# Kernel tuning notes

Measured on AMD Instinct MI355X. Metric: run time of the kernel, lower is better.

Reference implementation:

```python
import jax, jax.numpy as jnp
import numpy as np

B, L, D = 4, 2048, 1024
H = 16
DH = D // H  # 64


def setup_inputs() -> dict:
    key = jax.random.key(0)
    ks = jax.random.split(key, 12)
    inp = {
        "key": jax.random.normal(ks[0], (B, L, D), jnp.float32),
        "value": jax.random.normal(ks[1], (B, L, D), jnp.float32),
        "query": jax.random.normal(ks[2], (B, L, D), jnp.float32),
        # causal mask: True = masked out (matches masked_fill semantics)
        "mask": jnp.broadcast_to(jnp.triu(jnp.ones((L, L), jnp.bool_), k=1), (B, L, L)),
        "Wk": jax.random.normal(ks[3], (D, D), jnp.float32) * 0.02,
        "bk": jnp.zeros((D,), jnp.float32),
        "Wv": jax.random.normal(ks[4], (D, D), jnp.float32) * 0.02,
        "bv": jnp.zeros((D,), jnp.float32),
        "Wq": jax.random.normal(ks[5], (D, D), jnp.float32) * 0.02,
        "bq": jnp.zeros((D,), jnp.float32),
        "Wo": jax.random.normal(ks[6], (D, D), jnp.float32) * 0.02,
        "bo": jnp.zeros((D,), jnp.float32),
    }
    return inp


def _split_heads(x):
    # [B, L, D] -> [B, H, L, DH]
    b, l, _ = x.shape
    return x.reshape(b, l, H, DH).transpose(0, 2, 1, 3)


def reference(key, value, query, mask, Wk, bk, Wv, bv, Wq, bq, Wo, bo):
    b, lq, _ = query.shape
    k_up = _split_heads(key @ Wk + bk)      # [B,H,Lk,DH]
    v_up = _split_heads(value @ Wv + bv)    # [B,H,Lk,DH]
    q_up = _split_heads(query @ Wq + bq) / jnp.sqrt(jnp.float32(DH))
    scores = jnp.einsum("bhqd,bhkd->bhqk", q_up, k_up)
    scores = jnp.where(mask[:, None, :, :], jnp.float32(-1e18), scores)
    attn = jax.nn.softmax(scores, axis=-1)  # dropout = identity (eval)
    ctx = jnp.einsum("bhqk,bhkd->bhqd", attn, v_up)
    ctx = ctx.transpose(0, 2, 1, 3).reshape(b, lq, H * DH)
    output = ctx @ Wo + bo                  # [B,Lq,D]
    top_attn = attn[:, 0, :, :]             # [B,Lq,Lk]
    return output, top_attn
```

## Files before the change

### kernel.cpp

```cpp
#include <hip/hip_runtime.h>
#include <hip/hip_bf16.h>
#include <stdint.h>

typedef unsigned short u16;
typedef unsigned int u32;
typedef __attribute__((ext_vector_type(8))) short bf16x8;
typedef __attribute__((ext_vector_type(4))) float f32x4;
typedef __attribute__((address_space(1))) unsigned int as1u;
typedef __attribute__((address_space(3))) unsigned int as3u;

#define DEV __device__ __forceinline__

DEV u16 f2bf(float f) {
  union { float f; unsigned u; } v; v.f = f;
  unsigned r = v.u + 0x7FFFu + ((v.u >> 16) & 1u);
  return (u16)(r >> 16);
}

DEV u32 cvtpk(float lo, float hi) {
  u32 r;
  asm("v_cvt_pk_bf16_f32 %0, %1, %2" : "=v"(r) : "v"(lo), "v"(hi));
  return r;
}

DEV void gl_lds16(const void* g, void* l) {
  __builtin_amdgcn_global_load_lds(
      reinterpret_cast<as1u*>(reinterpret_cast<uintptr_t>(g)),
      reinterpret_cast<as3u*>(reinterpret_cast<uintptr_t>(l)), 16, 0, 0);
}

DEV int swzh(int r, int c) { return r * 64 + (c ^ ((r & 7) << 3)); }
DEV int swzf(int r, int c) { return r * 64 + (c ^ ((r & 7) << 2)); }

DEV int xcdswz512(int bid) { return ((bid & 7) << 6) | (bid >> 3); }

__global__ __launch_bounds__(256) void cvt3_k(const float* __restrict__ I0,
                                              const float* __restrict__ I1,
                                              const float* __restrict__ I2,
                                              u16* __restrict__ O0,
                                              u16* __restrict__ O1,
                                              u16* __restrict__ O2) {
  const int z = blockIdx.z;
  const float* in = z == 0 ? I0 : z == 1 ? I1 : I2;
  u16* out = z == 0 ? O0 : z == 1 ? O1 : O2;
  const int idx = blockIdx.x * 256 + threadIdx.x;
#pragma unroll
  for (int j = 0; j < 8; ++j) {
    const int i = j * 262144 + idx;
    float4 x = ((const float4*)in)[i];
    uint2 p;
    p.x = cvtpk(x.x, x.y);
    p.y = cvtpk(x.z, x.w);
    ((uint2*)out)[i] = p;
  }
}

__global__ __launch_bounds__(256) void wtrans4_k(
    const float* __restrict__ W0, const float* __restrict__ W1,
    const float* __restrict__ W2, const float* __restrict__ W3,
    u16* __restrict__ T0, u16* __restrict__ T1, u16* __restrict__ T2,
    u16* __restrict__ T3) {
  const int z = blockIdx.z;
  const float* W = z == 0 ? W0 : z == 1 ? W1 : z == 2 ? W2 : W3;
  u16* Wt = z == 0 ? T0 : z == 1 ? T1 : z == 2 ? T2 : T3;
  __shared__ float t[64][65];
  const int tid = threadIdx.x;
  const int n0 = blockIdx.x * 64, k0 = blockIdx.y * 64;
  const int c = tid & 63, r4 = tid >> 6;
#pragma unroll
  for (int i = 0; i < 16; ++i) {
    int r = r4 * 16 + i;
    t[r][c] = W[(size_t)(k0 + r) * 1024 + n0 + c];
  }
  __syncthreads();
#pragma unroll
  for (int i = 0; i < 16; ++i) {
    int r = r4 * 16 + i;
    Wt[(size_t)(n0 + r) * 1024 + k0 + c] = f2bf(t[c][r]);
  }
}

__global__ __launch_bounds__(256) void qkvgemm_k(
    const u16* __restrict__ Akey, const u16* __restrict__ Aval,
    const u16* __restrict__ Aqry, const u16* __restrict__ BtK,
    const u16* __restrict__ BtV, const u16* __restrict__ BtQ,
    const float* __restrict__ bk, const float* __restrict__ bv,
    const float* __restrict__ bq, u16* __restrict__ Kup, u16* __restrict__ Vt,
    u16* __restrict__ Qup, float qscale) {
  constexpr int K = 1024;
  const int z = blockIdx.z;
  const u16* Ah = z == 0 ? Akey : z == 1 ? Aval : Aqry;
  const u16* Bt = z == 0 ? BtK : z == 1 ? BtV : BtQ;
  const float* bias = z == 0 ? bk : z == 1 ? bv : bq;
  u16* Cp = z == 0 ? Kup : z == 1 ? Vt : Qup;
  const float scale = z == 2 ? qscale : 1.0f;

  __shared__ alignas(16) char smem[65536];

  const int tid = threadIdx.x;
  const int lane = tid & 63, wid = tid >> 6;
  const int swz = xcdswz512(blockIdx.x);
  const int brow = (swz >> 3) * 128;
  const int bcol = (swz & 7) * 128;
  const int wr = (wid >> 1) * 64, wc = (wid & 1) * 64;

  f32x4 acc[4][4] = {};

  auto stage = [&](int kt, int buf) {
#pragma unroll
    for (int i = 0; i < 4; ++i) {
      int row = i * 32 + (tid >> 3);
      const int sc = ((tid & 7) ^ (row & 7)) << 3;
      gl_lds16(Ah + (size_t)(brow + row) * K + kt + sc,
               smem + buf * 32768 + i * 4096 + wid * 1024);
      gl_lds16(Bt + (size_t)(bcol + row) * K + kt + sc,
               smem + buf * 32768 + 16384 + i * 4096 + wid * 1024);
    }
  };

  stage(0, 0);
  __syncthreads();

  int cur = 0;
  for (int kt = 0; kt < K; kt += 64) {
    if (kt + 64 < K) stage(kt + 64, cur ^ 1);
    const u16* Ash = (const u16*)(smem + cur * 32768);
    const u16* Bs = (const u16*)(smem + cur * 32768 + 16384);
#pragma unroll
    for (int kk = 0; kk < 2; ++kk) {
      const int kcol = kk * 32 + (lane >> 4) * 8;
      bf16x8 a[4], bfr[4];
#pragma unroll
      for (int m = 0; m < 4; ++m)
        a[m] = *(const bf16x8*)(Ash + swzh(wr + m * 16 + (lane & 15), kcol));
#pragma unroll
      for (int n = 0; n < 4; ++n)
        bfr[n] = *(const bf16x8*)(Bs + swzh(wc + n * 16 + (lane & 15), kcol));
#pragma unroll
      for (int m = 0; m < 4; ++m)
#pragma unroll
        for (int n = 0; n < 4; ++n)
          acc[m][n] = __builtin_amdgcn_mfma_f32_16x16x32_bf16(
              a[m], bfr[n], acc[m][n], 0, 0, 0);
    }
    __syncthreads();
    cur ^= 1;
  }

  const int g = lane >> 4;
  if (z == 1) {
    u16* T = (u16*)smem;
#pragma unroll
    for (int m = 0; m < 4; ++m) {
      const int row0 = wr + m * 16 + g * 4;
#pragma unroll
      for (int n = 0; n < 4; ++n) {
        const int col = wc + n * 16 + (lane & 15);
        const float bv2 = bias[bcol + col];
        uint2 p;
        p.x = cvtpk(acc[m][n][0] + bv2, acc[m][n][1] + bv2);
        p.y = cvtpk(acc[m][n][2] + bv2, acc[m][n][3] + bv2);
        *(uint2*)((char*)T + col * 256 + ((row0 * 2) ^ ((col & 7) << 4))) = p;
      }
    }
    __syncthreads();
    const int bI = brow >> 11, l0 = brow & 2047;
#pragma unroll
    for (int i = 0; i < 8; ++i) {
      const int rr = i * 16 + (tid >> 4);
      const int xb = (tid & 15) * 16;
      uint4 v = *(uint4*)((char*)T + rr * 256 + (xb ^ ((rr & 7) << 4)));
      const int colg = bcol + rr;
      const int hh = colg >> 6, dh = colg & 63;
      *(uint4*)(&Cp[((size_t)((bI << 4) + hh) * 64 + dh) * 2048 + l0 +
                    (xb >> 1)]) = v;
    }
  } else {
#pragma unroll
    for (int m = 0; m < 4; ++m) {
      const int row0 = brow + wr + m * 16 + (g << 2);
#pragma unroll
      for (int n = 0; n < 4; ++n) {
        const int col = bcol + wc + n * 16 + (lane & 15);
        const float bv2 = bias[col];
        const int h = col >> 6, dh = col & 63;
#pragma unroll
        for (int r = 0; r < 4; ++r) {
          const int row = row0 + r;
          const float val = (acc[m][n][r] + bv2) * scale;
          const int b = row >> 11, l = row & 2047;
          Cp[((size_t)((b << 4) + h) * 2048 + l) * 64 + dh] = f2bf(val);
        }
      }
    }
  }
}

__global__ __launch_bounds__(256) void outgemm_k(const u16* __restrict__ Ah,
                                                 const u16* __restrict__ Bt,
                                                 const float* __restrict__ bias,
                                                 float* __restrict__ Cp) {
  constexpr int K = 1024;
  __shared__ alignas(16) char smem[65536];

  const int tid = threadIdx.x;
  const int lane = tid & 63, wid = tid >> 6;
  const int swz = xcdswz512(blockIdx.x);
  const int brow = (swz >> 3) * 128;
  const int bcol = (swz & 7) * 128;
  const int wr = (wid >> 1) * 64, wc = (wid & 1) * 64;

  f32x4 acc[4][4] = {};

  auto stage = [&](int kt, int buf) {
#pragma unroll
    for (int i = 0; i < 4; ++i) {
      int row = i * 32 + (tid >> 3);
      const int sc = ((tid & 7) ^ (row & 7)) << 3;
      gl_lds16(Ah + (size_t)(brow + row) * K + kt + sc,
               smem + buf * 32768 + i * 4096 + wid * 1024);
      gl_lds16(Bt + (size_t)(bcol + row) * K + kt + sc,
               smem + buf * 32768 + 16384 + i * 4096 + wid * 1024);
    }
  };

  stage(0, 0);
  __syncthreads();

  int cur = 0;
  for (int kt = 0; kt < K; kt += 64) {
    if (kt + 64 < K) stage(kt + 64, cur ^ 1);
    const u16* Ash = (const u16*)(smem + cur * 32768);
    const u16* Bs = (const u16*)(smem + cur * 32768 + 16384);
#pragma unroll
    for (int kk = 0; kk < 2; ++kk) {
      const int kcol = kk * 32 + (lane >> 4) * 8;
      bf16x8 a[4], bfr[4];
#pragma unroll
      for (int m = 0; m < 4; ++m)
        a[m] = *(const bf16x8*)(Ash + swzh(wr + m * 16 + (lane & 15), kcol));
#pragma unroll
      for (int n = 0; n < 4; ++n)
        bfr[n] = *(const bf16x8*)(Bs + swzh(wc + n * 16 + (lane & 15), kcol));
#pragma unroll
      for (int m = 0; m < 4; ++m)
#pragma unroll
        for (int n = 0; n < 4; ++n)
          acc[m][n] = __builtin_amdgcn_mfma_f32_16x16x32_bf16(
              a[m], bfr[n], acc[m][n], 0, 0, 0);
    }
    __syncthreads();
    cur ^= 1;
  }

#pragma unroll
  for (int m = 0; m < 4; ++m) {
    const int row0 = brow + wr + m * 16 + ((lane >> 4) << 2);
#pragma unroll
    for (int n = 0; n < 4; ++n) {
      const int col = bcol + wc + n * 16 + (lane & 15);
      const float bv2 = bias[col];
#pragma unroll
      for (int r = 0; r < 4; ++r)
        Cp[(size_t)(row0 + r) * 1024 + col] = acc[m][n][r] + bv2;
    }
  }
}

__global__ __launch_bounds__(512, 6) void attn_k(const u16* __restrict__ Q,
                                                 const u16* __restrict__ K,
                                                 const u16* __restrict__ Vt,
                                                 u16* __restrict__ ctx,
                                                 float2* __restrict__ stats) {
  const int tid = threadIdx.x, lane = tid & 63, wid = tid >> 6;
  const int bh = blockIdx.x;
  const int qt = (int)(gridDim.y - 1) - (int)blockIdx.y;
  const int b = bh >> 4, h = bh & 15;
  const size_t base = (size_t)bh * 2048 * 64;

  __shared__ alignas(16) u16 Ks[2][4096], Vs[2][4096], Ps[8192];

  bf16x8 qf[2];
  {
    const u16* qp = Q + base +
                    (size_t)(qt * 128 + wid * 16 + (lane & 15)) * 64 +
                    ((lane >> 4) << 3);
    qf[0] = *(const bf16x8*)(qp);
    qf[1] = *(const bf16x8*)(qp + 32);
  }

  const int srow = tid >> 3;
  const int scol = ((tid & 7) ^ (srow & 7)) << 3;

  f32x4 acc_o[4] = {};
  float m_run = -1e30f, l_run = 0.f;
  const int q = qt * 128 + wid * 16 + (lane & 15);
  const int qminw = qt * 128 + wid * 16;
  const int qmaxw = qminw + 15;
  const int g = lane >> 4;
  const int rmask7 = lane & 7;

  const int NT = 2 * qt + 2;

  gl_lds16(K + base + (size_t)srow * 64 + scol, (char*)Ks + tid * 16);
  gl_lds16(Vt + base + (size_t)srow * 2048 + scol, (char*)Vs + tid * 16);
  __syncthreads();

  int cur = 0;
  for (int kt = 0; kt < NT; ++kt) {
    if (kt < NT - 1) {
      gl_lds16(K + base + (size_t)((kt + 1) * 64 + srow) * 64 + scol,
               (char*)Ks + (cur ^ 1) * 8192 + tid * 16);
      gl_lds16(Vt + base + (size_t)srow * 2048 + (kt + 1) * 64 + scol,
               (char*)Vs + (cur ^ 1) * 8192 + tid * 16);
    }

    if (kt * 64 <= qmaxw) {
      f32x4 s[4] = {};
#pragma unroll
      for (int kk = 0; kk < 2; ++kk) {
        const int kcb = kk * 64 + g * 16;
#pragma unroll
        for (int n = 0; n < 4; ++n) {
          const int row = n * 16 + (lane & 15);
          bf16x8 kf = *(const bf16x8*)((char*)Ks + cur * 8192 + row * 128 +
                                       (kcb ^ (rmask7 << 4)));
          s[n] = __builtin_amdgcn_mfma_f32_16x16x32_bf16(kf, qf[kk], s[n],
                                                         0, 0, 0);
        }
      }

      if (kt * 64 + 63 > qminw) {
        const int kb = kt * 64 + g * 4;
#pragma unroll
        for (int n = 0; n < 4; ++n)
#pragma unroll
          for (int r = 0; r < 4; ++r)
            if (kb + n * 16 + r > q) s[n][r] = -1e30f;
      }

      float mx = s[0][0];
#pragma unroll
      for (int n = 0; n < 4; ++n)
#pragma unroll
        for (int r = 0; r < 4; ++r) mx = fmaxf(mx, s[n][r]);
      mx = fmaxf(mx, __shfl_xor(mx, 16, 64));
      mx = fmaxf(mx, __shfl_xor(mx, 32, 64));

      if (__any(mx - m_run > 8.0f)) {
        const float mn = fmaxf(m_run, mx);
        const float alpha = exp2f(m_run - mn);
        m_run = mn;
        l_run *= alpha;
#pragma unroll
        for (int r = 0; r < 4; ++r) {
          const float ar = __shfl(alpha, (g << 2) + r, 64);
#pragma unroll
          for (int n = 0; n < 4; ++n) acc_o[n][r] *= ar;
        }
      }

      float rs = 0.f;
#pragma unroll
      for (int n = 0; n < 4; ++n)
#pragma unroll
        for (int r = 0; r < 4; ++r) {
          const float pv = exp2f(s[n][r] - m_run);
          s[n][r] = pv;
          rs += pv;
        }
      rs += __shfl_xor(rs, 16, 64);
      rs += __shfl_xor(rs, 32, 64);
      l_run += rs;

#pragma unroll
      for (int n = 0; n < 4; ++n) {
        union { u32 w[2]; uint2 u; } pk;
        pk.w[0] = cvtpk(s[n][0], s[n][1]);
        pk.w[1] = cvtpk(s[n][2], s[n][3]);
        *(uint2*)((char*)Ps + wid * 2048 + (lane & 15) * 128 +
                  ((n * 32 + g * 8) ^ (rmask7 << 4))) = pk.u;
      }
      asm volatile("s_waitcnt lgkmcnt(0)" ::: "memory");

#pragma unroll
      for (int kk = 0; kk < 2; ++kk) {
        const int kcb = kk * 64 + g * 16;
        bf16x8 pf = *(const bf16x8*)((char*)Ps + wid * 2048 +
                                     (lane & 15) * 128 + (kcb ^ (rmask7 << 4)));
#pragma unroll
        for (int n = 0; n < 4; ++n) {
          const int row = n * 16 + (lane & 15);
          bf16x8 vf = *(const bf16x8*)((char*)Vs + cur * 8192 + row * 128 +
                                       (kcb ^ (rmask7 << 4)));
          acc_o[n] = __builtin_amdgcn_mfma_f32_16x16x32_bf16(pf, vf, acc_o[n],
                                                             0, 0, 0);
        }
      }
    }
    __syncthreads();
    cur ^= 1;
  }

  float linv[4];
#pragma unroll
  for (int r = 0; r < 4; ++r)
    linv[r] = 1.0f / __shfl(l_run, (g << 2) + r, 64);
#pragma unroll
  for (int r = 0; r < 4; ++r) {
    const int qo = qt * 128 + wid * 16 + (g << 2) + r;
#pragma unroll
    for (int n = 0; n < 4; ++n) {
      const int dh = n * 16 + (lane & 15);
      ctx[((size_t)(b * 2048 + qo)) * 1024 + h * 64 + dh] =
          f2bf(acc_o[n][r] * linv[r]);
    }
  }
  if (h == 0 && g == 0)
    stats[b * 2048 + q] = make_float2(m_run, l_run);
}

__global__ __launch_bounds__(256) void probs_k(const u16* __restrict__ Q,
                                               const u16* __restrict__ K,
                                               const float2* __restrict__ stats,
                                               float* __restrict__ out) {
  const int tid = threadIdx.x, lane = tid & 63, wid = tid >> 6;
  const int kt2 = blockIdx.x, qt = blockIdx.y, b = blockIdx.z;
  const int q0 = qt * 64, c0 = kt2 * 128;
  float* ot = out + ((size_t)b * 2048 + q0) * 2048 + c0;

  if (c0 > q0 + 63) {
    const float4 z = make_float4(0.f, 0.f, 0.f, 0.f);
#pragma unroll
    for (int i = 0; i < 8; ++i) {
      const int idx = i * 256 + tid;
      *(float4*)(ot + (size_t)(idx >> 5) * 2048 + ((idx & 31) << 2)) = z;
    }
    return;
  }

  __shared__ alignas(16) u16 Qs[4096], Ks2[8192];
  const size_t base = (size_t)(b * 16) * 2048 * 64;
#pragma unroll
  for (int i = 0; i < 2; ++i) {
    int row = i * 32 + (tid >> 3);
    gl_lds16(Q + base + (size_t)(q0 + row) * 64 + (((tid & 7) ^ (row & 7)) << 3),
             (char*)Qs + i * 4096 + wid * 1024);
  }
#pragma unroll
  for (int i = 0; i < 4; ++i) {
    int row = i * 32 + (tid >> 3);
    gl_lds16(K + base + (size_t)(c0 + row) * 64 + (((tid & 7) ^ (row & 7)) << 3),
             (char*)Ks2 + i * 4096 + wid * 1024);
  }
  __syncthreads();

  f32x4 s[8] = {};
#pragma unroll
  for (int kk = 0; kk < 2; ++kk) {
    const int kc = kk * 32 + (lane >> 4) * 8;
    bf16x8 aq = *(const bf16x8*)(Qs + swzh(wid * 16 + (lane & 15), kc));
#pragma unroll
    for (int n = 0; n < 8; ++n) {
      bf16x8 bk = *(const bf16x8*)(Ks2 + swzh(n * 16 + (lane & 15), kc));
      s[n] = __builtin_amdgcn_mfma_f32_16x16x32_bf16(aq, bk, s[n], 0, 0, 0);
    }
  }

#pragma unroll
  for (int r = 0; r < 4; ++r) {
    const int q = q0 + wid * 16 + ((lane >> 4) << 2) + r;
    const float2 st = stats[b * 2048 + q];
    const float rl = 1.0f / st.y;
#pragma unroll
    for (int n = 0; n < 8; ++n) {
      const int kp = c0 + n * 16 + (lane & 15);
      out[((size_t)b * 2048 + q) * 2048 + kp] =
          (kp <= q) ? exp2f(s[n][r] - st.x) * rl : 0.f;
    }
  }
}

extern "C" void kernel_launch(void* const* d_in, const int* in_sizes, int n_in,
                              void* d_out, int out_size, void* d_ws,
                              size_t ws_size, hipStream_t stream) {
  (void)in_sizes; (void)n_in; (void)out_size; (void)ws_size;
  const float* key = (const float*)d_in[0];
  const float* value = (const float*)d_in[1];
  const float* query = (const float*)d_in[2];
  const float* Wk = (const float*)d_in[4];
  const float* bk = (const float*)d_in[5];
  const float* Wv = (const float*)d_in[6];
  const float* bv = (const float*)d_in[7];
  const float* Wq = (const float*)d_in[8];
  const float* bq = (const float*)d_in[9];
  const float* Wo = (const float*)d_in[10];
  const float* bo = (const float*)d_in[11];

  char* ws = (char*)d_ws;
  u16* WtK = (u16*)(ws);
  u16* WtV = (u16*)(ws + (2u << 20));
  u16* WtQ = (u16*)(ws + (4u << 20));
  u16* WtO = (u16*)(ws + (6u << 20));
  u16* Kup = (u16*)(ws + (8u << 20));
  u16* Qup = (u16*)(ws + (24u << 20));
  u16* Vt  = (u16*)(ws + (40u << 20));
  u16* ctx = (u16*)(ws + (56u << 20));
  float2* stats = (float2*)(ws + (72u << 20));
  u16* Akb = (u16*)(ws + (76u << 20));
  u16* Avb = (u16*)(ws + (92u << 20));
  u16* Aqb = (u16*)(ws + (108u << 20));

  wtrans4_k<<<dim3(16, 16, 4), 256, 0, stream>>>(Wk, Wv, Wq, Wo, WtK, WtV,
                                                 WtQ, WtO);
  cvt3_k<<<dim3(1024, 1, 3), 256, 0, stream>>>(key, value, query, Akb, Avb,
                                               Aqb);

  const float qscale = 0.125f * 1.44269504088896340736f;
  qkvgemm_k<<<dim3(512, 1, 3), 256, 0, stream>>>(
      Akb, Avb, Aqb, WtK, WtV, WtQ, bk, bv, bq, Kup, Vt, Qup, qscale);

  attn_k<<<dim3(64, 16), 512, 0, stream>>>(Qup, Kup, Vt, ctx, stats);

  float* out = (float*)d_out;
  probs_k<<<dim3(16, 32, 4), 256, 0, stream>>>(Qup, Kup, stats,
                                               out + (size_t)8388608);

  outgemm_k<<<512, 256, 0, stream>>>(ctx, WtO, bo, out);
}
```

Measured before the change: 206.3 us.

## Use 128-wide KV tiles in attention and compute row sums via MFMA

```diff
diff --git a/kernel.cpp b/kernel.cpp
--- a/kernel.cpp
+++ b/kernel.cpp
@@ -30,7 +30,6 @@
 }
 
 DEV int swzh(int r, int c) { return r * 64 + (c ^ ((r & 7) << 3)); }
-DEV int swzf(int r, int c) { return r * 64 + (c ^ ((r & 7) << 2)); }
 
 DEV int xcdswz512(int bid) { return ((bid & 7) << 6) | (bid >> 3); }
 
@@ -267,18 +266,18 @@
   }
 }
 
-__global__ __launch_bounds__(512, 6) void attn_k(const u16* __restrict__ Q,
+__global__ __launch_bounds__(512, 4) void attn_k(const u16* __restrict__ Q,
                                                  const u16* __restrict__ K,
                                                  const u16* __restrict__ Vt,
                                                  u16* __restrict__ ctx,
                                                  float2* __restrict__ stats) {
   const int tid = threadIdx.x, lane = tid & 63, wid = tid >> 6;
   const int bh = blockIdx.x;
-  const int qt = (int)(gridDim.y - 1) - (int)blockIdx.y;
+  const int qt = 15 - (int)blockIdx.y;
   const int b = bh >> 4, h = bh & 15;
   const size_t base = (size_t)bh * 2048 * 64;
 
-  __shared__ alignas(16) u16 Ks[2][4096], Vs[2][4096], Ps[8192];
+  __shared__ alignas(16) u16 Ks[2][8192], Vs[2][8192], Ps[8192];
 
   bf16x8 qf[2];
   {
@@ -288,136 +287,147 @@
     qf[0] = *(const bf16x8*)(qp);
     qf[1] = *(const bf16x8*)(qp + 32);
   }
-
-  const int srow = tid >> 3;
-  const int scol = ((tid & 7) ^ (srow & 7)) << 3;
-
-  f32x4 acc_o[4] = {};
-  float m_run = -1e30f, l_run = 0.f;
+  bf16x8 ones;
+#pragma unroll
+  for (int i = 0; i < 8; ++i) ones[i] = (short)0x3F80;
+
+  const int srowK = tid >> 3;
+  const int scolK = ((tid & 7) ^ (srowK & 7)) << 3;
+  const int srowV = tid >> 4;
+  const int scolV = ((tid & 15) ^ (srowV & 7)) << 3;
+  auto stage = [&](int kt, int buf) {
+#pragma unroll
+    for (int i = 0; i < 2; ++i)
+      gl_lds16(K + base + (size_t)(kt * 128 + i * 64 + srowK) * 64 + scolK,
+               (char*)Ks + buf * 16384 + i * 8192 + tid * 16);
+#pragma unroll
+    for (int i = 0; i < 2; ++i)
+      gl_lds16(Vt + base + (size_t)(i * 32 + srowV) * 2048 + kt * 128 + scolV,
+               (char*)Vs + buf * 16384 + i * 8192 + tid * 16);
+  };
+
+  f32x4 acc_o[4] = {}, acc_l = {};
+  float m_run = -1e30f;
   const int q = qt * 128 + wid * 16 + (lane & 15);
-  const int qminw = qt * 128 + wid * 16;
-  const int qmaxw = qminw + 15;
   const int g = lane >> 4;
-  const int rmask7 = lane & 7;
-
-  const int NT = 2 * qt + 2;
-
-  gl_lds16(K + base + (size_t)srow * 64 + scol, (char*)Ks + tid * 16);
-  gl_lds16(Vt + base + (size_t)srow * 2048 + scol, (char*)Vs + tid * 16);
+  const int l7 = lane & 7;
+
+  stage(0, 0);
   __syncthreads();
 
   int cur = 0;
-  for (int kt = 0; kt < NT; ++kt) {
-    if (kt < NT - 1) {
-      gl_lds16(K + base + (size_t)((kt + 1) * 64 + srow) * 64 + scol,
-               (char*)Ks + (cur ^ 1) * 8192 + tid * 16);
-      gl_lds16(Vt + base + (size_t)srow * 2048 + (kt + 1) * 64 + scol,
-               (char*)Vs + (cur ^ 1) * 8192 + tid * 16);
-    }
-
-    if (kt * 64 <= qmaxw) {
-      f32x4 s[4] = {};
-#pragma unroll
-      for (int kk = 0; kk < 2; ++kk) {
-        const int kcb = kk * 64 + g * 16;
+  for (int kt = 0; kt <= qt; ++kt) {
+    if (kt < qt) stage(kt + 1, cur ^ 1);
+
+    f32x4 s[8] = {};
+#pragma unroll
+    for (int kk = 0; kk < 2; ++kk) {
+      const int kcb = kk * 64 + g * 16;
+#pragma unroll
+      for (int n2 = 0; n2 < 8; ++n2) {
+        const int row = n2 * 16 + (lane & 15);
+        bf16x8 kf = *(const bf16x8*)((char*)Ks + cur * 16384 + row * 128 +
+                                     (kcb ^ ((row & 7) << 4)));
+        s[n2] = __builtin_amdgcn_mfma_f32_16x16x32_bf16(kf, qf[kk], s[n2],
+                                                        0, 0, 0);
+      }
+    }
+
+    if (kt == qt) {
+      const int kb = kt * 128 + g * 4;
+#pragma unroll
+      for (int n2 = 0; n2 < 8; ++n2)
+#pragma unroll
+        for (int r = 0; r < 4; ++r)
+          if (kb + n2 * 16 + r > q) s[n2][r] = -1e30f;
+    }
+
+    float mn0 = fmaxf(fmaxf(fmaxf(s[0][0], s[0][1]), fmaxf(s[0][2], s[0][3])),
+                      fmaxf(fmaxf(s[1][0], s[1][1]), fmaxf(s[1][2], s[1][3])));
+    float mn1 = fmaxf(fmaxf(fmaxf(s[2][0], s[2][1]), fmaxf(s[2][2], s[2][3])),
+                      fmaxf(fmaxf(s[3][0], s[3][1]), fmaxf(s[3][2], s[3][3])));
+    float mn2 = fmaxf(fmaxf(fmaxf(s[4][0], s[4][1]), fmaxf(s[4][2], s[4][3])),
+                      fmaxf(fmaxf(s[5][0], s[5][1]), fmaxf(s[5][2], s[5][3])));
+    float mn3 = fmaxf(fmaxf(fmaxf(s[6][0], s[6][1]), fmaxf(s[6][2], s[6][3])),
+                      fmaxf(fmaxf(s[7][0], s[7][1]), fmaxf(s[7][2], s[7][3])));
+    float mx = fmaxf(fmaxf(mn0, mn1), fmaxf(mn2, mn3));
+    mx = fmaxf(mx, __shfl_xor(mx, 16, 64));
+    mx = fmaxf(mx, __shfl_xor(mx, 32, 64));
+
+    if (__any(mx - m_run > 8.0f)) {
+      const float mn = fmaxf(m_run, mx);
+      const float alpha = exp2f(m_run - mn);
+      m_run = mn;
+#pragma unroll
+      for (int r = 0; r < 4; ++r) {
+        const float ar = __shfl(alpha, (g << 2) + r, 64);
+        acc_l[r] *= ar;
+#pragma unroll
+        for (int n = 0; n < 4; ++n) acc_o[n][r] *= ar;
+      }
+    }
+
+#pragma unroll
+    for (int n2 = 0; n2 < 8; ++n2)
+#pragma unroll
+      for (int r = 0; r < 4; ++r) s[n2][r] = exp2f(s[n2][r] - m_run);
+
+#pragma unroll
+    for (int hf = 0; hf < 2; ++hf) {
+#pragma unroll
+      for (int n3 = 0; n3 < 4; ++n3) {
+        const int n2 = hf * 4 + n3;
+        union { u32 w[2]; uint2 u; } pk;
+        pk.w[0] = cvtpk(s[n2][0], s[n2][1]);
+        pk.w[1] = cvtpk(s[n2][2], s[n2][3]);
+        *(uint2*)((char*)Ps + wid * 2048 + (lane & 15) * 128 +
+                  ((n3 * 32 + g * 8) ^ (l7 << 4))) = pk.u;
+      }
+#pragma unroll
+      for (int kk2 = 0; kk2 < 2; ++kk2) {
+        bf16x8 pf = *(const bf16x8*)((char*)Ps + wid * 2048 +
+                                     (lane & 15) * 128 +
+                                     ((kk2 * 64 + g * 16) ^ (l7 << 4)));
+        const int kvb = hf * 128 + kk2 * 64 + g * 16;
 #pragma unroll
         for (int n = 0; n < 4; ++n) {
-          const int row = n * 16 + (lane & 15);
-          bf16x8 kf = *(const bf16x8*)((char*)Ks + cur * 8192 + row * 128 +
-                                       (kcb ^ (rmask7 << 4)));
-          s[n] = __builtin_amdgcn_mfma_f32_16x16x32_bf16(kf, qf[kk], s[n],
-                                                         0, 0, 0);
-        }
-      }
-
-      if (kt * 64 + 63 > qminw) {
-        const int kb = kt * 64 + g * 4;
-#pragma unroll
-        for (int n = 0; n < 4; ++n)
-#pragma unroll
-          for (int r = 0; r < 4; ++r)
-            if (kb + n * 16 + r > q) s[n][r] = -1e30f;
-      }
-
-      float mx = s[0][0];
-#pragma unroll
-      for (int n = 0; n < 4; ++n)
-#pragma unroll
-        for (int r = 0; r < 4; ++r) mx = fmaxf(mx, s[n][r]);
-      mx = fmaxf(mx, __shfl_xor(mx, 16, 64));
-      mx = fmaxf(mx, __shfl_xor(mx, 32, 64));
-
-      if (__any(mx - m_run > 8.0f)) {
-        const float mn = fmaxf(m_run, mx);
-        const float alpha = exp2f(m_run - mn);
-        m_run = mn;
-        l_run *= alpha;
-#pragma unroll
-        for (int r = 0; r < 4; ++r) {
-          const float ar = __shfl(alpha, (g << 2) + r, 64);
-#pragma unroll
-          for (int n = 0; n < 4; ++n) acc_o[n][r] *= ar;
-        }
-      }
-
-      float rs = 0.f;
-#pragma unroll
-      for (int n = 0; n < 4; ++n)
-#pragma unroll
-        for (int r = 0; r < 4; ++r) {
-          const float pv = exp2f(s[n][r] - m_run);
-          s[n][r] = pv;
-          rs += pv;
-        }
-      rs += __shfl_xor(rs, 16, 64);
-      rs += __shfl_xor(rs, 32, 64);
-      l_run += rs;
-
-#pragma unroll
-      for (int n = 0; n < 4; ++n) {
-        union { u32 w[2]; uint2 u; } pk;
-        pk.w[0] = cvtpk(s[n][0], s[n][1]);
-        pk.w[1] = cvtpk(s[n][2], s[n][3]);
-        *(uint2*)((char*)Ps + wid * 2048 + (lane & 15) * 128 +
-                  ((n * 32 + g * 8) ^ (rmask7 << 4))) = pk.u;
-      }
-      asm volatile("s_waitcnt lgkmcnt(0)" ::: "memory");
-
-#pragma unroll
-      for (int kk = 0; kk < 2; ++kk) {
-        const int kcb = kk * 64 + g * 16;
-        bf16x8 pf = *(const bf16x8*)((char*)Ps + wid * 2048 +
-                                     (lane & 15) * 128 + (kcb ^ (rmask7 << 4)));
-#pragma unroll
-        for (int n = 0; n < 4; ++n) {
-          const int row = n * 16 + (lane & 15);
-          bf16x8 vf = *(const bf16x8*)((char*)Vs + cur * 8192 + row * 128 +
-                                       (kcb ^ (rmask7 << 4)));
+          const int dh = n * 16 + (lane & 15);
+          bf16x8 vf = *(const bf16x8*)((char*)Vs + cur * 16384 + dh * 256 +
+                                       (kvb ^ ((dh & 7) << 4)));
           acc_o[n] = __builtin_amdgcn_mfma_f32_16x16x32_bf16(pf, vf, acc_o[n],
                                                              0, 0, 0);
         }
+        acc_l = __builtin_amdgcn_mfma_f32_16x16x32_bf16(pf, ones, acc_l,
+                                                        0, 0, 0);
       }
     }
     __syncthreads();
     cur ^= 1;
   }
 
-  float linv[4];
-#pragma unroll
-  for (int r = 0; r < 4; ++r)
-    linv[r] = 1.0f / __shfl(l_run, (g << 2) + r, 64);
 #pragma unroll
   for (int r = 0; r < 4; ++r) {
+    const float linv = 1.0f / acc_l[r];
     const int qo = qt * 128 + wid * 16 + (g << 2) + r;
 #pragma unroll
     for (int n = 0; n < 4; ++n) {
       const int dh = n * 16 + (lane & 15);
       ctx[((size_t)(b * 2048 + qo)) * 1024 + h * 64 + dh] =
-          f2bf(acc_o[n][r] * linv[r]);
-    }
-  }
-  if (h == 0 && g == 0)
-    stats[b * 2048 + q] = make_float2(m_run, l_run);
+          f2bf(acc_o[n][r] * linv);
+    }
+  }
+  if (h == 0) {
+    float mr[4];
+#pragma unroll
+    for (int r = 0; r < 4; ++r) mr[r] = __shfl(m_run, (g << 2) + r, 64);
+    if ((lane & 15) == 0) {
+#pragma unroll
+      for (int r = 0; r < 4; ++r) {
+        const int qo = qt * 128 + wid * 16 + (g << 2) + r;
+        stats[b * 2048 + qo] = make_float2(mr[r], acc_l[r]);
+      }
+    }
+  }
 }
 
 __global__ __launch_bounds__(256) void probs_k(const u16* __restrict__ Q,
```

Result: no change. 203.6 us (-1.3%).
